# Optimization experiments

Measured on AMD Instinct MI355X. Metric: run time of the kernel, lower is better.

Reference implementation:

```python
import jax, jax.numpy as jnp
import numpy as np

NUM_GRAPHS = 512  # number of segments (graphs) in the batch


def setup_inputs() -> dict:
    key = jax.random.key(0)
    k1, k2, k3, k4, k5, k6 = jax.random.split(key, 6)
    N, Din, D, H = 100000, 1024, 64, 32
    x = jax.random.normal(k1, (N, Din), dtype=jnp.float32)
    batch = jnp.sort(jax.random.randint(k2, (N,), 0, NUM_GRAPHS)).astype(jnp.int64)
    W_enc = jax.random.normal(k3, (D, Din), dtype=jnp.float32) * (1.0 / np.sqrt(Din))
    b_enc = jax.random.normal(k4, (D,), dtype=jnp.float32) * 0.01
    W_gate = jax.random.normal(k5, (H, D), dtype=jnp.float32) * (1.0 / np.sqrt(D))
    b_gate = jax.random.normal(k6, (H,), dtype=jnp.float32) * 0.01
    return {"x": x, "batch": batch, "W_enc": W_enc, "b_enc": b_enc,
            "W_gate": W_gate, "b_gate": b_gate}


def reference(x, batch, W_enc, b_enc, W_gate, b_gate):
    B = NUM_GRAPHS
    batch = batch.astype(jnp.int32)
    # shared encoder: [N, Din] -> [N, D]
    xe = jnp.dot(x, W_enc.T) + b_enc
    # all 32 heads' scalar gates at once: [N, H]
    gate = jnp.dot(xe, W_gate.T) + b_gate
    # segment-wise (per-graph) stable softmax over nodes, per head
    gmax = jax.ops.segment_max(gate, batch, num_segments=B)          # [B, H]
    g = jnp.exp(gate - gmax[batch])                                   # [N, H]
    gsum = jax.ops.segment_sum(g, batch, num_segments=B)             # [B, H]
    alpha = g / gsum[batch]                                           # [N, H]
    # scatter-weighted sum: out[b,h,d] = sum_{n in graph b} alpha[n,h]*xe[n,d]
    weighted = alpha[:, :, None] * xe[:, None, :]                     # [N, H, D]
    pooled = jax.ops.segment_sum(weighted, batch, num_segments=B)    # [B, H, D]
    # concat over heads (head i occupies cols [i*D, (i+1)*D)) then ReLU
    return jax.nn.relu(pooled.reshape(B, -1))
```

## Files before the change

### kernel.cpp

```cpp
#include <hip/hip_runtime.h>


typedef short bf16x8 __attribute__((ext_vector_type(8)));
typedef float f32x4 __attribute__((ext_vector_type(4)));

#define NUM_GRAPHS 512
#define DIN 1024
#define DENC 64
#define NH 32
#define NB 96
#define LDA 72
#define LDB 72

__device__ __forceinline__ unsigned short f2bf(float f) {
    unsigned int u = __float_as_uint(f);
    return (unsigned short)((u + 0x7fffu + ((u >> 16) & 1u)) >> 16);
}
__device__ __forceinline__ void split2(float f, unsigned short& h, unsigned short& l) {
    unsigned int u = __float_as_uint(f);
    unsigned int hb = (u + 0x7fffu + ((u >> 16) & 1u)) >> 16;
    h = (unsigned short)hb;
    float hf = __uint_as_float(hb << 16);
    l = f2bf(f - hf);
}

__device__ __forceinline__ int clampseg(int v) {
    return v < 0 ? 0 : (v >= NUM_GRAPHS ? NUM_GRAPHS - 1 : v);
}

__global__ void k_prep(const int* __restrict__ batch, int* __restrict__ seg, int N,
                       const float* __restrict__ W,
                       const float* __restrict__ Wg,
                       const float* __restrict__ bg,
                       const float* __restrict__ be,
                       unsigned short* __restrict__ Wh,
                       unsigned short* __restrict__ Wl,
                       float* __restrict__ bcomb,
                       int nseg_blocks, int nconv_blocks)
{
    const int blk = blockIdx.x;
    const int tid = threadIdx.x;
    if (blk < nseg_blocks) {
        int n = blk * 256 + tid;
        if (n >= N) return;
        int bc = clampseg(batch[n]);
        if (n == 0) {
            for (int j = 0; j <= bc; ++j) seg[j] = 0;
            int bl = clampseg(batch[N - 1]);
            for (int j = bl + 1; j <= NUM_GRAPHS; ++j) seg[j] = N;
        } else {
            int bp = clampseg(batch[n - 1]);
            for (int j = bp + 1; j <= bc; ++j) seg[j] = n;
        }
    } else if (blk < nseg_blocks + nconv_blocks) {
        int idx = ((blk - nseg_blocks) * 256 + tid) * 4;
        float4 v = *(const float4*)(W + idx);
        ushort4 h4, l4;
        split2(v.x, h4.x, l4.x);
        split2(v.y, h4.y, l4.y);
        split2(v.z, h4.z, l4.z);
        split2(v.w, h4.w, l4.w);
        *(ushort4*)(Wh + idx) = h4;
        *(ushort4*)(Wl + idx) = l4;
    } else {
        __shared__ float wgr[DENC];
        const int j = blk - nseg_blocks - nconv_blocks;
        if (tid < DENC) wgr[tid] = Wg[j * DENC + tid];
        __syncthreads();
        const int k0 = tid * 4;
        float4 a = {0.f, 0.f, 0.f, 0.f};
        for (int d = 0; d < DENC; ++d) {
            float w = wgr[d];
            float4 v = *(const float4*)(W + d * DIN + k0);
            a.x += w * v.x; a.y += w * v.y; a.z += w * v.z; a.w += w * v.w;
        }
        ushort4 h4, l4;
        split2(a.x, h4.x, l4.x);
        split2(a.y, h4.y, l4.y);
        split2(a.z, h4.z, l4.z);
        split2(a.w, h4.w, l4.w);
        *(ushort4*)(Wh + (DENC + j) * DIN + k0) = h4;
        *(ushort4*)(Wl + (DENC + j) * DIN + k0) = l4;
        if (tid == 0) {
            float s = bg[j];
            for (int d = 0; d < DENC; ++d) s += wgr[d] * be[d];
            bcomb[j] = s;
        }
    }
}

__global__ __launch_bounds__(256, 2) void k_gemm(
    const float* __restrict__ x,
    const unsigned short* __restrict__ Wh,
    const unsigned short* __restrict__ Wl,
    const float* __restrict__ b_enc,
    const float* __restrict__ bcomb,
    float* __restrict__ xe,
    float* __restrict__ gate,
    int N)
{
    __shared__ unsigned short Ah[128 * LDA], Al[128 * LDA];
    __shared__ unsigned short Bh[NB * LDB],  Bl[NB * LDB];

    const int tid  = threadIdx.x;
    const int lane = tid & 63;
    const int wv   = tid >> 6;
    const long brow = (long)blockIdx.x * 128;

    f32x4 acc[2][6];
    #pragma unroll
    for (int i = 0; i < 2; ++i)
        #pragma unroll
        for (int j = 0; j < 6; ++j) acc[i][j] = (f32x4){0.f, 0.f, 0.f, 0.f};

    const int ar0 = tid >> 4;
    const int ac4 = (tid & 15) * 4;
    const int br0 = tid >> 3;
    const int bc8 = (tid & 7) * 8;
    const int fr  = lane & 15;
    const int fq  = lane >> 4;

    float4 va0[8], va1[8];
    uint4  vbh[3], vbl[3];

    auto loadA = [&](float4 (&va)[8], int kc) {
        #pragma unroll
        for (int i = 0; i < 8; ++i) {
            int row = ar0 + 16 * i;
            long gr = brow + row;
            va[i] = (gr < N) ? *(const float4*)(x + gr * DIN + kc + ac4)
                             : (float4){0.f, 0.f, 0.f, 0.f};
        }
    };
    auto loadB = [&](int kc) {
        #pragma unroll
        for (int i = 0; i < 3; ++i) {
            int row = br0 + 32 * i;
            vbh[i] = *(const uint4*)(Wh + row * DIN + kc + bc8);
            vbl[i] = *(const uint4*)(Wl + row * DIN + kc + bc8);
        }
    };
    auto stageA = [&](float4 (&va)[8]) {
        #pragma unroll
        for (int i = 0; i < 8; ++i) {
            int row = ar0 + 16 * i;
            ushort4 h4, l4;
            split2(va[i].x, h4.x, l4.x);
            split2(va[i].y, h4.y, l4.y);
            split2(va[i].z, h4.z, l4.z);
            split2(va[i].w, h4.w, l4.w);
            *(ushort4*)&Ah[row * LDA + ac4] = h4;
            *(ushort4*)&Al[row * LDA + ac4] = l4;
        }
    };
    auto stageB = [&]() {
        #pragma unroll
        for (int i = 0; i < 3; ++i) {
            int row = br0 + 32 * i;
            *(uint4*)&Bh[row * LDB + bc8] = vbh[i];
            *(uint4*)&Bl[row * LDB + bc8] = vbl[i];
        }
    };
    auto mfmaPhase = [&]() {
        #pragma unroll
        for (int kk = 0; kk < 64; kk += 32) {
            bf16x8 ah[2], al[2];
            #pragma unroll
            for (int rt = 0; rt < 2; ++rt) {
                int o = (wv * 32 + rt * 16 + fr) * LDA + fq * 8 + kk;
                ah[rt] = *(const bf16x8*)&Ah[o];
                al[rt] = *(const bf16x8*)&Al[o];
            }
            #pragma unroll
            for (int ct = 0; ct < 6; ++ct) {
                int o = (ct * 16 + fr) * LDB + fq * 8 + kk;
                bf16x8 bh = *(const bf16x8*)&Bh[o];
                bf16x8 bl = *(const bf16x8*)&Bl[o];
                #pragma unroll
                for (int rt = 0; rt < 2; ++rt) {
                    acc[rt][ct] = __builtin_amdgcn_mfma_f32_16x16x32_bf16(ah[rt], bh, acc[rt][ct], 0, 0, 0);
                    acc[rt][ct] = __builtin_amdgcn_mfma_f32_16x16x32_bf16(ah[rt], bl, acc[rt][ct], 0, 0, 0);
                    acc[rt][ct] = __builtin_amdgcn_mfma_f32_16x16x32_bf16(al[rt], bh, acc[rt][ct], 0, 0, 0);
                }
            }
        }
    };

    loadA(va0, 0);
    loadA(va1, 64);
    loadB(0);

    for (int k0 = 0; k0 < DIN; k0 += 128) {
        stageA(va0);
        stageB();
        __syncthreads();
        if (k0 + 128 < DIN) loadA(va0, k0 + 128);
        loadB(k0 + 64);
        mfmaPhase();
        __syncthreads();

        stageA(va1);
        stageB();
        __syncthreads();
        if (k0 + 192 < DIN) loadA(va1, k0 + 192);
        if (k0 + 128 < DIN) loadB(k0 + 128);
        mfmaPhase();
        __syncthreads();
    }

    float bv[4], bcv[2];
    #pragma unroll
    for (int ct = 0; ct < 4; ++ct) bv[ct] = b_enc[ct * 16 + fr];
    #pragma unroll
    for (int j = 0; j < 2; ++j) bcv[j] = bcomb[j * 16 + fr];
    #pragma unroll
    for (int rt = 0; rt < 2; ++rt) {
        #pragma unroll
        for (int r = 0; r < 4; ++r) {
            long row = brow + wv * 32 + rt * 16 + fq * 4 + r;
            if (row < N) {
                float* o = xe + row * DENC;
                #pragma unroll
                for (int ct = 0; ct < 4; ++ct)
                    o[ct * 16 + fr] = acc[rt][ct][r] + bv[ct];
                float* g = gate + row * NH;
                #pragma unroll
                for (int j = 0; j < 2; ++j)
                    g[j * 16 + fr] = acc[rt][4 + j][r] + bcv[j];
            }
        }
    }
}

__global__ __launch_bounds__(256) void k_pool(
    const float* __restrict__ xe,
    const float* __restrict__ gate,
    const int* __restrict__ seg,
    float* __restrict__ out,
    int N)
{
    __shared__ float xs[64 * 68];
    __shared__ float gs[64 * 36];
    const int tid = threadIdx.x;
    const int b = blockIdx.x;
    const int s = seg[b], e = seg[b + 1];
    const long ob = (long)b * (NH * DENC);
    if (e <= s) {
        for (int i = tid; i < NH * DENC; i += 256) out[ob + i] = 0.f;
        return;
    }
    const int rl = tid & 63;
    const int hq = tid >> 6;
    const int h0 = hq * 8;
    const int r0s = tid >> 4, c4 = (tid & 15) * 4;

    float m[8], pool[8], gp[8];
    #pragma unroll
    for (int j = 0; j < 8; ++j) { m[j] = -INFINITY; pool[j] = 0.f; gp[j] = 0.f; }

    float4 xv[4];
    float gv[8];
    auto load_chunk = [&](int base, int nrow) {
        #pragma unroll
        for (int i = 0; i < 4; ++i) {
            int row = r0s + 16 * i;
            xv[i] = (row < nrow)
                  ? *(const float4*)(xe + (long)(base + row) * DENC + c4)
                  : (float4){0.f, 0.f, 0.f, 0.f};
        }
        if (rl < nrow) {
            const float* g0 = gate + (long)(base + rl) * NH + h0;
            float4 a = *(const float4*)g0;
            float4 c = *(const float4*)(g0 + 4);
            gv[0] = a.x; gv[1] = a.y; gv[2] = a.z; gv[3] = a.w;
            gv[4] = c.x; gv[5] = c.y; gv[6] = c.z; gv[7] = c.w;
        } else {
            #pragma unroll
            for (int j = 0; j < 8; ++j) gv[j] = -INFINITY;
        }
    };

    load_chunk(s, min(64, e - s));

    for (int base = s; base < e; base += 64) {
        const int nrow = min(64, e - base);
        float cm[8];
        #pragma unroll
        for (int j = 0; j < 8; ++j) cm[j] = gv[j];
        #pragma unroll
        for (int off = 32; off > 0; off >>= 1)
            #pragma unroll
            for (int j = 0; j < 8; ++j) cm[j] = fmaxf(cm[j], __shfl_xor(cm[j], off));
        #pragma unroll
        for (int j = 0; j < 8; ++j) {
            if (cm[j] > m[j]) {
                float sc = (m[j] == -INFINITY) ? 0.f : __expf(m[j] - cm[j]);
                pool[j] *= sc;
                gp[j]   *= sc;
                m[j] = cm[j];
            }
        }
        float4 ga, gb;
        ga.x = __expf(gv[0] - m[0]); ga.y = __expf(gv[1] - m[1]);
        ga.z = __expf(gv[2] - m[2]); ga.w = __expf(gv[3] - m[3]);
        gb.x = __expf(gv[4] - m[4]); gb.y = __expf(gv[5] - m[5]);
        gb.z = __expf(gv[6] - m[6]); gb.w = __expf(gv[7] - m[7]);
        gp[0] += ga.x; gp[1] += ga.y; gp[2] += ga.z; gp[3] += ga.w;
        gp[4] += gb.x; gp[5] += gb.y; gp[6] += gb.z; gp[7] += gb.w;
        #pragma unroll
        for (int i = 0; i < 4; ++i)
            *(float4*)&xs[(r0s + 16 * i) * 68 + c4] = xv[i];
        *(float4*)&gs[rl * 36 + h0] = ga;
        *(float4*)&gs[rl * 36 + h0 + 4] = gb;
        int nb = base + 64;
        if (nb < e) load_chunk(nb, min(64, e - nb));
        __syncthreads();
        #pragma unroll 4
        for (int r2 = 0; r2 < nrow; ++r2) {
            float xvv = xs[r2 * 68 + rl];
            float4 g1 = *(const float4*)&gs[r2 * 36 + h0];
            float4 g2 = *(const float4*)&gs[r2 * 36 + h0 + 4];
            pool[0] += g1.x * xvv; pool[1] += g1.y * xvv;
            pool[2] += g1.z * xvv; pool[3] += g1.w * xvv;
            pool[4] += g2.x * xvv; pool[5] += g2.y * xvv;
            pool[6] += g2.z * xvv; pool[7] += g2.w * xvv;
        }
        __syncthreads();
    }
    #pragma unroll
    for (int off = 32; off > 0; off >>= 1)
        #pragma unroll
        for (int j = 0; j < 8; ++j) gp[j] += __shfl_xor(gp[j], off);
    #pragma unroll
    for (int j = 0; j < 8; ++j) {
        float v = pool[j] / gp[j];
        out[ob + (h0 + j) * DENC + rl] = fmaxf(v, 0.f);
    }
}

extern "C" void kernel_launch(void* const* d_in, const int* in_sizes, int n_in,
                              void* d_out, int out_size, void* d_ws, size_t ws_size,
                              hipStream_t stream)
{
    const float* x      = (const float*)d_in[0];
    const int* batch    = (const int*)d_in[1];
    const float* W_enc  = (const float*)d_in[2];
    const float* b_enc  = (const float*)d_in[3];
    const float* W_gate = (const float*)d_in[4];
    const float* b_gate = (const float*)d_in[5];
    float* out = (float*)d_out;
    const int N = in_sizes[1];

    char* ws = (char*)d_ws;
    size_t off = 0;
    auto take = [&](size_t bytes) {
        char* p = ws + off;
        off += (bytes + 255) & ~(size_t)255;
        return p;
    };
    float* xe   = (float*)take((size_t)N * DENC * sizeof(float));
    float* gate = (float*)take((size_t)N * NH * sizeof(float));
    unsigned short* Wh = (unsigned short*)take((size_t)NB * DIN * 2);
    unsigned short* Wl = (unsigned short*)take((size_t)NB * DIN * 2);
    float* bcomb = (float*)take(NH * sizeof(float));
    int* seg = (int*)take((NUM_GRAPHS + 1) * sizeof(int));
    (void)ws_size; (void)n_in; (void)out_size;

    const int nseg_blocks  = (N + 255) / 256;
    const int nconv_blocks = (DENC * DIN) / 1024;
    k_prep<<<nseg_blocks + nconv_blocks + NH, 256, 0, stream>>>(
        batch, seg, N, W_enc, W_gate, b_gate, b_enc, Wh, Wl, bcomb, nseg_blocks, nconv_blocks);
    k_gemm<<<(N + 127) / 128, 256, 0, stream>>>(x, Wh, Wl, b_enc, bcomb, xe, gate, N);
    k_pool<<<NUM_GRAPHS, 256, 0, stream>>>(xe, gate, seg, out, N);
}
```

Measured before the change: 655.5 us.

## Shrink GEMM K-tile to 32 and raise occupancy to four blocks per CU

The encoder GEMM now uses a K-tile of 32 with a single register prefetch buffer instead of two 64-wide buffers, which shrinks the LDS tiles (LDA/LDB 40) and the register footprint. Launch bounds move from 2 to 4 blocks per CU so more waves can hide global-load latency. A-loads now have each thread read 16 contiguous floats of one row, and B-loads use narrower ushort4 accesses. In exchange there are twice as many barriers per K, less prefetch distance, and smaller per-thread loads.

Result: faster. 623.0 us (-4.9%).

```diff
diff --git a/kernel.cpp b/kernel.cpp
--- a/kernel.cpp
+++ b/kernel.cpp
@@ -9,8 +9,9 @@
 #define DENC 64
 #define NH 32
 #define NB 96
-#define LDA 72
-#define LDB 72
+#define BK 32
+#define LDA 40
+#define LDB 40
 
 __device__ __forceinline__ unsigned short f2bf(float f) {
     unsigned int u = __float_as_uint(f);
@@ -89,7 +90,7 @@
     }
 }
 
-__global__ __launch_bounds__(256, 2) void k_gemm(
+__global__ __launch_bounds__(256, 4) void k_gemm(
     const float* __restrict__ x,
     const unsigned short* __restrict__ Wh,
     const unsigned short* __restrict__ Wl,
@@ -113,97 +114,90 @@
         #pragma unroll
         for (int j = 0; j < 6; ++j) acc[i][j] = (f32x4){0.f, 0.f, 0.f, 0.f};
 
-    const int ar0 = tid >> 4;
-    const int ac4 = (tid & 15) * 4;
-    const int br0 = tid >> 3;
-    const int bc8 = (tid & 7) * 8;
+    const int arow = tid >> 1;
+    const int ac16 = (tid & 1) * 16;
     const int fr  = lane & 15;
     const int fq  = lane >> 4;
 
-    float4 va0[8], va1[8];
-    uint4  vbh[3], vbl[3];
-
-    auto loadA = [&](float4 (&va)[8], int kc) {
-        #pragma unroll
-        for (int i = 0; i < 8; ++i) {
-            int row = ar0 + 16 * i;
-            long gr = brow + row;
-            va[i] = (gr < N) ? *(const float4*)(x + gr * DIN + kc + ac4)
-                             : (float4){0.f, 0.f, 0.f, 0.f};
-        }
+    float4  va[4];
+    ushort4 vbh[3], vbl[3];
+
+    const long arowg = brow + arow;
+    const bool arok = (arowg < N);
+    const float* aptr = x + arowg * DIN + ac16;
+
+    auto loadA = [&](int kc) {
+        #pragma unroll
+        for (int i = 0; i < 4; ++i)
+            va[i] = arok ? *(const float4*)(aptr + kc + 4 * i)
+                         : (float4){0.f, 0.f, 0.f, 0.f};
     };
     auto loadB = [&](int kc) {
         #pragma unroll
         for (int i = 0; i < 3; ++i) {
-            int row = br0 + 32 * i;
-            vbh[i] = *(const uint4*)(Wh + row * DIN + kc + bc8);
-            vbl[i] = *(const uint4*)(Wl + row * DIN + kc + bc8);
-        }
-    };
-    auto stageA = [&](float4 (&va)[8]) {
-        #pragma unroll
-        for (int i = 0; i < 8; ++i) {
-            int row = ar0 + 16 * i;
+            int idx = tid + 256 * i;
+            int row = idx >> 3;
+            int c4  = (idx & 7) * 4;
+            vbh[i] = *(const ushort4*)(Wh + row * DIN + kc + c4);
+            vbl[i] = *(const ushort4*)(Wl + row * DIN + kc + c4);
+        }
+    };
+    auto stageA = [&]() {
+        #pragma unroll
+        for (int i = 0; i < 4; ++i) {
             ushort4 h4, l4;
             split2(va[i].x, h4.x, l4.x);
             split2(va[i].y, h4.y, l4.y);
             split2(va[i].z, h4.z, l4.z);
             split2(va[i].w, h4.w, l4.w);
-            *(ushort4*)&Ah[row * LDA + ac4] = h4;
-            *(ushort4*)&Al[row * LDA + ac4] = l4;
+            *(ushort4*)&Ah[arow * LDA + ac16 + 4 * i] = h4;
+            *(ushort4*)&Al[arow * LDA + ac16 + 4 * i] = l4;
         }
     };
     auto stageB = [&]() {
         #pragma unroll
         for (int i = 0; i < 3; ++i) {
-            int row = br0 + 32 * i;
-            *(uint4*)&Bh[row * LDB + bc8] = vbh[i];
-            *(uint4*)&Bl[row * LDB + bc8] = vbl[i];
+            int idx = tid + 256 * i;
+            int row = idx >> 3;
+            int c4  = (idx & 7) * 4;
+            *(ushort4*)&Bh[row * LDB + c4] = vbh[i];
+            *(ushort4*)&Bl[row * LDB + c4] = vbl[i];
         }
     };
     auto mfmaPhase = [&]() {
-        #pragma unroll
-        for (int kk = 0; kk < 64; kk += 32) {
-            bf16x8 ah[2], al[2];
+        bf16x8 ah[2], al[2];
+        #pragma unroll
+        for (int rt = 0; rt < 2; ++rt) {
+            int o = (wv * 32 + rt * 16 + fr) * LDA + fq * 8;
+            ah[rt] = *(const bf16x8*)&Ah[o];
+            al[rt] = *(const bf16x8*)&Al[o];
+        }
+        #pragma unroll
+        for (int ct = 0; ct < 6; ++ct) {
+            int o = (ct * 16 + fr) * LDB + fq * 8;
+            bf16x8 bh = *(const bf16x8*)&Bh[o];
+            bf16x8 bl = *(const bf16x8*)&Bl[o];
             #pragma unroll
             for (int rt = 0; rt < 2; ++rt) {
-                int o = (wv * 32 + rt * 16 + fr) * LDA + fq * 8 + kk;
-                ah[rt] = *(const bf16x8*)&Ah[o];
-                al[rt] = *(const bf16x8*)&Al[o];
+                acc[rt][ct] = __builtin_amdgcn_mfma_f32_16x16x32_bf16(ah[rt], bh, acc[rt][ct], 0, 0, 0);
+                acc[rt][ct] = __builtin_amdgcn_mfma_f32_16x16x32_bf16(ah[rt], bl, acc[rt][ct], 0, 0, 0);
+                acc[rt][ct] = __builtin_amdgcn_mfma_f32_16x16x32_bf16(al[rt], bh, acc[rt][ct], 0, 0, 0);
             }
-            #pragma unroll
-            for (int ct = 0; ct < 6; ++ct) {
-                int o = (ct * 16 + fr) * LDB + fq * 8 + kk;
-                bf16x8 bh = *(const bf16x8*)&Bh[o];
-                bf16x8 bl = *(const bf16x8*)&Bl[o];
-                #pragma unroll
-                for (int rt = 0; rt < 2; ++rt) {
-                    acc[rt][ct] = __builtin_amdgcn_mfma_f32_16x16x32_bf16(ah[rt], bh, acc[rt][ct], 0, 0, 0);
-                    acc[rt][ct] = __builtin_amdgcn_mfma_f32_16x16x32_bf16(ah[rt], bl, acc[rt][ct], 0, 0, 0);
-                    acc[rt][ct] = __builtin_amdgcn_mfma_f32_16x16x32_bf16(al[rt], bh, acc[rt][ct], 0, 0, 0);
-                }
-            }
-        }
-    };
-
-    loadA(va0, 0);
-    loadA(va1, 64);
+        }
+    };
+
+    loadA(0);
     loadB(0);
 
-    for (int k0 = 0; k0 < DIN; k0 += 128) {
-        stageA(va0);
+    for (int k0 = 0; k0 < DIN; k0 += BK) {
+        stageA();
         stageB();
         __syncthreads();
-        if (k0 + 128 < DIN) loadA(va0, k0 + 128);
-        loadB(k0 + 64);
-        mfmaPhase();
-        __syncthreads();
-
-        stageA(va1);
-        stageB();
-        __syncthreads();
-        if (k0 + 192 < DIN) loadA(va1, k0 + 192);
-        if (k0 + 128 < DIN) loadB(k0 + 128);
+        const int kn = k0 + BK;
+        if (kn < DIN) {
+            loadA(kn);
+            loadB(kn);
+        }
         mfmaPhase();
         __syncthreads();
     }
```
